# Performance work log

Hardware: AMD Instinct MI355X
Metric: run time of the kernel (lower is better)

Reference implementation:

```python
import jax, jax.numpy as jnp
import numpy as np

EPS = 1e-5
SLOPE = 0.2

def _knn_idx(x, k):
    # x: (B, N, C) -> idx (B, N, k), k nearest neighbors by squared L2 (incl. self)
    xx = jnp.sum(x * x, axis=-1)                      # (B, N)
    inner = jnp.einsum('bnc,bmc->bnm', x, x)          # (B, N, N)
    pd = -xx[:, :, None] + 2.0 * inner - xx[:, None, :]  # = -||xi-xj||^2
    return jax.lax.top_k(pd, k)[1]                    # (B, N, k)

def _bn(h, gamma, beta, axes):
    mean = jnp.mean(h, axis=axes, keepdims=True)
    var = jnp.var(h, axis=axes, keepdims=True)
    hn = (h - mean) * jax.lax.rsqrt(var + EPS)
    shape = [1] * h.ndim
    shape[-1] = h.shape[-1]
    return hn * gamma.reshape(shape) + beta.reshape(shape)

def _lrelu(h):
    return jnp.where(h >= 0, h, SLOPE * h)

def _edge_conv(x, k, W, gamma, beta):
    # x: (B, N, C); EdgeConv: knn -> gather -> [nb-x, x] -> 1x1 conv -> BN -> LeakyReLU -> max over k
    idx = _knn_idx(x, k)                                   # (B, N, k)
    nb = jax.vmap(lambda xb, ib: xb[ib])(x, idx)           # (B, N, k, C)
    xc = jnp.broadcast_to(x[:, :, None, :], nb.shape)
    feat = jnp.concatenate([nb - xc, xc], axis=-1)         # (B, N, k, 2C)
    h = jnp.einsum('bnkc,oc->bnko', feat, W)               # 1x1 conv, no bias
    h = _lrelu(_bn(h, gamma, beta, axes=(0, 1, 2)))
    return jnp.max(h, axis=2)                              # (B, N, O)

def setup_inputs() -> dict:
    key = jax.random.key(0)
    ks = jax.random.split(key, 16)
    B, N, feat_dim = 8, 2048, 1024
    def w(k_, o, i):
        # kaiming-uniform-ish init for 1x1 conv
        bound = 1.0 / np.sqrt(i)
        return jax.random.uniform(k_, (o, i), jnp.float32, -bound, bound)
    inp = {
        'x': jax.random.normal(ks[0], (B, N, 3), jnp.float32),
        'W1': w(ks[1], 64, 6),   'g1': jnp.ones((64,)),  'b1': jnp.zeros((64,)),
        'W2': w(ks[2], 64, 128), 'g2': jnp.ones((64,)),  'b2': jnp.zeros((64,)),
        'W3': w(ks[3], 128, 128),'g3': jnp.ones((128,)), 'b3': jnp.zeros((128,)),
        'W4': w(ks[4], 256, 256),'g4': jnp.ones((256,)), 'b4': jnp.zeros((256,)),
        'W5': w(ks[5], feat_dim, 512), 'g5': jnp.ones((feat_dim,)), 'b5': jnp.zeros((feat_dim,)),
        'k': 20,
    }
    return inp

def reference(x, W1, g1, b1, W2, g2, b2, W3, g3, b3, W4, g4, b4, W5, g5, b5, k):
    x1 = _edge_conv(x,  k, W1, g1, b1)   # (B, N, 64)
    x2 = _edge_conv(x1, k, W2, g2, b2)   # (B, N, 64)
    x3 = _edge_conv(x2, k, W3, g3, b3)   # (B, N, 128)
    x4 = _edge_conv(x3, k, W4, g4, b4)   # (B, N, 256)
    xc = jnp.concatenate([x1, x2, x3, x4], axis=-1)   # (B, N, 512)
    h = jnp.einsum('bnc,oc->bno', xc, W5)             # conv5 (1x1, no bias)
    h = _lrelu(_bn(h, g5, b5, axes=(0, 1)))           # BatchNorm1d + LeakyReLU
    out = jnp.max(h, axis=1)                          # global max over points
    return out[:, None, :]                            # (B, 1, feat_dim)
```

## Files before the change

kernel.cpp:

```cpp
#include <hip/hip_runtime.h>
#include <hip/hip_bf16.h>

#define BB 8
#define NN 2048
#define KK 20
#define KSEL 32
#define SCAP 256

typedef __attribute__((ext_vector_type(8))) short short8v;
typedef __attribute__((ext_vector_type(4))) float f32x4;

__global__ __launch_bounds__(256) void norms_k(const float* __restrict__ xin, int C, int stride,
                                               float* __restrict__ xx) {
  int p = blockIdx.x * 256 + threadIdx.x;
  if (p >= BB * NN) return;
  const float* r = xin + (size_t)p * stride;
  double s = 0.0;
  for (int c = 0; c < C; ++c) { double v = (double)r[c]; s += v * v; }
  xx[p] = (float)s;
}

__device__ __forceinline__ void bitsel_fallback(unsigned (&u)[32], int lane,
                                                int* __restrict__ outp)
{
  unsigned long long lmask = (1ull << lane) - 1ull;
  unsigned T = 0;
  bool exact = false;
  for (int b = 31; b >= 0; --b) {
    unsigned Tp = T | (1u << b);
    int cnt = 0;
#pragma unroll
    for (int q = 0; q < 32; ++q)
      cnt += __popcll(__ballot(u[q] >= Tp));
    if (cnt >= KSEL) {
      T = Tp;
      if (cnt == KSEL) { exact = true; break; }
    }
  }
  int cnt = 0;
#pragma unroll
  for (int q = 0; q < 32; ++q) {
    bool take = exact ? (u[q] >= T) : (u[q] > T);
    unsigned long long m = __ballot(take);
    if (take) outp[cnt + __popcll(m & lmask)] = lane + 64 * q;
    cnt += __popcll(m);
  }
  if (!exact) {
    int tneed = KSEL - cnt;
#pragma unroll
    for (int q = 0; q < 32; ++q) {
      if (tneed > 0) {
        bool eq = (u[q] == T);
        unsigned long long m = __ballot(eq);
        int before = __popcll(m & lmask);
        if (eq && before < tneed) outp[cnt + before] = lane + 64 * q;
        int c = __popcll(m);
        int used = c < tneed ? c : tneed;
        cnt += used; tneed -= used;
      }
    }
  }
}

__device__ __forceinline__ void thresel32(unsigned (&u)[32], int lane,
                                          unsigned* __restrict__ cv, int* __restrict__ ci,
                                          int* __restrict__ outp)
{
  unsigned long long lmask = (1ull << lane) - 1ull;
  unsigned lm = u[0];
#pragma unroll
  for (int q = 1; q < 32; ++q) lm = u[q] > lm ? u[q] : lm;
  unsigned T = 0;
  for (int b = 31; b >= 0; --b) {
    unsigned Tp = T | (1u << b);
    int c = __popcll(__ballot(lm >= Tp));
    if (c >= 32) { T = Tp; if (c == 32) break; }
  }
  int n0 = 0;
#pragma unroll
  for (int q = 0; q < 32; ++q) n0 += __popcll(__ballot(u[q] >= T));
  if (n0 <= SCAP) {
    int cnt = 0;
#pragma unroll
    for (int q = 0; q < 32; ++q) {
      bool take = u[q] >= T;
      unsigned long long m = __ballot(take);
      if (take) {
        int pos = cnt + __popcll(m & lmask);
        cv[pos] = u[q];
        ci[pos] = lane + 64 * q;
      }
      cnt += __popcll(m);
    }
    for (int i = lane; i < n0; i += 64) {
      unsigned vi = cv[i];
      int rank = 0;
      for (int j = 0; j < n0; ++j) {
        unsigned vj = cv[j];
        rank += (vj > vi || (vj == vi && j < i)) ? 1 : 0;
      }
      if (rank < KSEL) outp[rank] = ci[i];
    }
  } else {
    bitsel_fallback(u, lane, outp);
  }
}

__global__ __launch_bounds__(256) void knn3_k(const float* __restrict__ xin,
                                              int* __restrict__ cand)
{
  int t = threadIdx.x;
  int wv = t >> 6, lane = t & 63;
  const int BPB = NN / 16;
  int b = blockIdx.x / BPB;
  int p0 = (blockIdx.x % BPB) * 16;
  __shared__ float xs[3][NN];
  __shared__ unsigned cvs[4][SCAP];
  __shared__ int cis[4][SCAP];
  const float* xb = xin + (size_t)b * NN * 3;
  for (int e = t; e < NN * 3; e += 256) xs[e % 3][e / 3] = xb[e];
  __syncthreads();
  for (int rr = 0; rr < 4; ++rr) {
    int row = p0 + wv * 4 + rr;
    float xi0 = xs[0][row], xi1 = xs[1][row], xi2 = xs[2][row];
    unsigned u[32];
#pragma unroll
    for (int q = 0; q < 32; ++q) {
      int j = lane + 64 * q;
      float d0 = xi0 - xs[0][j], d1 = xi1 - xs[1][j], d2 = xi2 - xs[2][j];
      float v = -(d0 * d0 + d1 * d1 + d2 * d2);
      unsigned bb = __float_as_uint(v);
      u[q] = bb ^ (((unsigned)((int)bb >> 31)) | 0x80000000u);
    }
    thresel32(u, lane, cvs[wv], cis[wv], cand + ((size_t)(b * NN + row)) * KSEL);
  }
}

__global__ __launch_bounds__(512) void pdmfma_k(
    const unsigned short* __restrict__ Ah, const unsigned short* __restrict__ Al,
    int lda, long long az,
    float* __restrict__ D, const float* __restrict__ xx, int Kd)
{
  __shared__ unsigned short AsH[128 * 64];
  __shared__ unsigned short AsL[128 * 64];
  __shared__ unsigned short BsH[128 * 64];
  __shared__ unsigned short BsL[128 * 64];
  int z = blockIdx.z;
  const unsigned short* Ahb = Ah + az * z;
  const unsigned short* Alb = Al + az * z;
  float* Db = D + (size_t)NN * NN * z;
  const float* xxb = xx + (size_t)NN * z;
  int t = threadIdx.x;
  int w = t >> 6, lane = t & 63;
  int wm = w >> 2, wn = w & 3;
  int i0 = blockIdx.x * 128, j0 = blockIdx.y * 128;
  int fr = lane & 15, fg = lane >> 4;
  int srow = t >> 3;
  int scol = (t & 7) * 8;
  f32x4 acc[4][2] = {};
  for (int k0 = 0; k0 < Kd; k0 += 64) {
    short8v vah[2], valo[2], vbh[2], vbl[2];
#pragma unroll
    for (int rr = 0; rr < 2; ++rr) {
      int row = srow + rr * 64;
      vah[rr]  = *(const short8v*)(Ahb + (size_t)(i0 + row) * lda + k0 + scol);
      valo[rr] = *(const short8v*)(Alb + (size_t)(i0 + row) * lda + k0 + scol);
      vbh[rr]  = *(const short8v*)(Ahb + (size_t)(j0 + row) * lda + k0 + scol);
      vbl[rr]  = *(const short8v*)(Alb + (size_t)(j0 + row) * lda + k0 + scol);
    }
    __syncthreads();
#pragma unroll
    for (int rr = 0; rr < 2; ++rr) {
      int row = srow + rr * 64;
      int sw = (row * 64 + scol) ^ ((row & 7) << 3);
      *(short8v*)&AsH[sw] = vah[rr];
      *(short8v*)&AsL[sw] = valo[rr];
      *(short8v*)&BsH[sw] = vbh[rr];
      *(short8v*)&BsL[sw] = vbl[rr];
    }
    __syncthreads();
#pragma unroll
    for (int kk = 0; kk < 2; ++kk) {
      short8v ah[4], al[4], bh[2], bl[2];
      int kb = kk * 32 + fg * 8;
#pragma unroll
      for (int m = 0; m < 4; ++m) {
        int ar = wm * 64 + m * 16 + fr;
        int ai = (ar * 64 + kb) ^ ((ar & 7) << 3);
        ah[m] = *(const short8v*)&AsH[ai];
        al[m] = *(const short8v*)&AsL[ai];
      }
#pragma unroll
      for (int n = 0; n < 2; ++n) {
        int br = wn * 32 + n * 16 + fr;
        int bi = (br * 64 + kb) ^ ((br & 7) << 3);
        bh[n] = *(const short8v*)&BsH[bi];
        bl[n] = *(const short8v*)&BsL[bi];
      }
#pragma unroll
      for (int m = 0; m < 4; ++m)
#pragma unroll
        for (int n = 0; n < 2; ++n) {
          acc[m][n] = __builtin_amdgcn_mfma_f32_16x16x32_bf16(ah[m], bh[n], acc[m][n], 0, 0, 0);
          acc[m][n] = __builtin_amdgcn_mfma_f32_16x16x32_bf16(ah[m], bl[n], acc[m][n], 0, 0, 0);
          acc[m][n] = __builtin_amdgcn_mfma_f32_16x16x32_bf16(al[m], bh[n], acc[m][n], 0, 0, 0);
        }
    }
    __syncthreads();
  }
#pragma unroll
  for (int m = 0; m < 4; ++m) {
    float xi[4];
#pragma unroll
    for (int j = 0; j < 4; ++j) xi[j] = xxb[i0 + wm * 64 + m * 16 + fg * 4 + j];
#pragma unroll
    for (int n = 0; n < 2; ++n) {
      float xj = xxb[j0 + wn * 32 + n * 16 + fr];
#pragma unroll
      for (int j = 0; j < 4; ++j)
        Db[(size_t)(i0 + wm * 64 + m * 16 + fg * 4 + j) * NN +
           j0 + wn * 32 + n * 16 + fr] = 2.f * acc[m][n][j] - xi[j] - xj;
    }
  }
}

__global__ __launch_bounds__(512) void gemm_fb_k(
    const unsigned short* __restrict__ Ah, const unsigned short* __restrict__ Al, int lda,
    const unsigned short* __restrict__ Bh, const unsigned short* __restrict__ Bl, int ldb,
    float* __restrict__ C, int ldc, int Kd)
{
  __shared__ unsigned short AsH[128 * 64];
  __shared__ unsigned short AsL[128 * 64];
  __shared__ unsigned short BsH[128 * 64];
  __shared__ unsigned short BsL[128 * 64];
  int t = threadIdx.x;
  int w = t >> 6, lane = t & 63;
  int wm = w >> 2, wn = w & 3;
  int i0 = blockIdx.x * 128, j0 = blockIdx.y * 128;
  int fr = lane & 15, fg = lane >> 4;
  int srow = t >> 3;
  int scol = (t & 7) * 8;
  f32x4 acc[4][2] = {};
  for (int k0 = 0; k0 < Kd; k0 += 64) {
    short8v vah[2], valo[2], vbh[2], vbl[2];
#pragma unroll
    for (int rr = 0; rr < 2; ++rr) {
      int row = srow + rr * 64;
      vah[rr]  = *(const short8v*)(Ah + (size_t)(i0 + row) * lda + k0 + scol);
      valo[rr] = *(const short8v*)(Al + (size_t)(i0 + row) * lda + k0 + scol);
      vbh[rr]  = *(const short8v*)(Bh + (size_t)(j0 + row) * ldb + k0 + scol);
      vbl[rr]  = *(const short8v*)(Bl + (size_t)(j0 + row) * ldb + k0 + scol);
    }
    __syncthreads();
#pragma unroll
    for (int rr = 0; rr < 2; ++rr) {
      int row = srow + rr * 64;
      int sw = (row * 64 + scol) ^ ((row & 7) << 3);
      *(short8v*)&AsH[sw] = vah[rr];
      *(short8v*)&AsL[sw] = valo[rr];
      *(short8v*)&BsH[sw] = vbh[rr];
      *(short8v*)&BsL[sw] = vbl[rr];
    }
    __syncthreads();
#pragma unroll
    for (int kk = 0; kk < 2; ++kk) {
      short8v ah[4], al[4], bh[2], bl[2];
      int kb = kk * 32 + fg * 8;
#pragma unroll
      for (int m = 0; m < 4; ++m) {
        int ar = wm * 64 + m * 16 + fr;
        int ai = (ar * 64 + kb) ^ ((ar & 7) << 3);
        ah[m] = *(const short8v*)&AsH[ai];
        al[m] = *(const short8v*)&AsL[ai];
      }
#pragma unroll
      for (int n = 0; n < 2; ++n) {
        int br = wn * 32 + n * 16 + fr;
        int bi = (br * 64 + kb) ^ ((br & 7) << 3);
        bh[n] = *(const short8v*)&BsH[bi];
        bl[n] = *(const short8v*)&BsL[bi];
      }
#pragma unroll
      for (int m = 0; m < 4; ++m)
#pragma unroll
        for (int n = 0; n < 2; ++n) {
          acc[m][n] = __builtin_amdgcn_mfma_f32_16x16x32_bf16(ah[m], bh[n], acc[m][n], 0, 0, 0);
          acc[m][n] = __builtin_amdgcn_mfma_f32_16x16x32_bf16(ah[m], bl[n], acc[m][n], 0, 0, 0);
          acc[m][n] = __builtin_amdgcn_mfma_f32_16x16x32_bf16(al[m], bh[n], acc[m][n], 0, 0, 0);
        }
    }
    __syncthreads();
  }
#pragma unroll
  for (int m = 0; m < 4; ++m)
#pragma unroll
    for (int n = 0; n < 2; ++n)
#pragma unroll
      for (int j = 0; j < 4; ++j)
        C[(size_t)(i0 + wm * 64 + m * 16 + fg * 4 + j) * ldc +
          j0 + wn * 32 + n * 16 + fr] = acc[m][n][j];
}

__global__ __launch_bounds__(256) void topk32_k(const float* __restrict__ dist, int row0,
                                                int* __restrict__ cand)
{
  int wv = threadIdx.x >> 6;
  int row = blockIdx.x * 4 + wv;
  int lane = threadIdx.x & 63;
  const float* d = dist + (size_t)row * NN;
  unsigned u[32];
#pragma unroll
  for (int q = 0; q < 32; ++q) {
    unsigned b = __float_as_uint(d[lane + 64 * q]);
    unsigned mk = ((unsigned)((int)b >> 31)) | 0x80000000u;
    u[q] = b ^ mk;
  }
  __shared__ unsigned cvs[4][SCAP];
  __shared__ int cis[4][SCAP];
  thresel32(u, lane, cvs[wv], cis[wv], cand + (size_t)(row0 + row) * KSEL);
}

template <int C>
__global__ __launch_bounds__(256) void refine4_k(const float* __restrict__ xin, int stride,
                                                 const int* __restrict__ cand,
                                                 int* __restrict__ idxout)
{
  int t = threadIdx.x;
  int w = t >> 6, lane = t & 63;
  int p = blockIdx.x * 4 + w;
  int b = p >> 11;
  __shared__ float xi[4][C < 4 ? 4 : C];
  __shared__ double Lval[4][KSEL];
  __shared__ int Lidx[4][KSEL];
#pragma unroll
  for (int c = lane; c < C; c += 64) xi[w][c] = xin[(size_t)p * stride + c];
  __syncthreads();
  int m = lane >> 1, h = lane & 1;
  int q = cand[(size_t)p * KSEL + m];
  const float* xr = xin + (size_t)(b * NN + q) * stride;
  double s;
  if constexpr (C >= 8) {
    constexpr int half = C >> 1;
    int c0 = h * half;
    float4 v[half / 4];
#pragma unroll
    for (int i = 0; i < half / 4; ++i) v[i] = *(const float4*)(xr + c0 + 4 * i);
    double a0 = 0.0, a1 = 0.0, a2 = 0.0, a3 = 0.0;
#pragma unroll
    for (int i = 0; i < half / 4; ++i) {
      float4 xv = *(const float4*)(&xi[w][c0 + 4 * i]);
      double d0 = (double)xv.x - (double)v[i].x;
      double d1 = (double)xv.y - (double)v[i].y;
      double d2 = (double)xv.z - (double)v[i].z;
      double d3 = (double)xv.w - (double)v[i].w;
      a0 += d0 * d0; a1 += d1 * d1; a2 += d2 * d2; a3 += d3 * d3;
    }
    s = (a0 + a1) + (a2 + a3);
  } else {
    s = 0.0;
#pragma unroll
    for (int c = h; c < C; c += 2) {
      double d = (double)xi[w][c] - (double)xr[c];
      s += d * d;
    }
  }
  s += __shfl_xor(s, 1);
  if (h == 0) { Lval[w][m] = -s; Lidx[w][m] = q; }
  __syncthreads();
  int mm = lane & 31;
  double vm = Lval[w][mm];
  int im = Lidx[w][mm];
  int rank = 0;
#pragma unroll
  for (int j = 0; j < KSEL; ++j) {
    double vj = Lval[w][j];
    int ij = Lidx[w][j];
    rank += (vj > vm || (vj == vm && ij < im)) ? 1 : 0;
  }
  if (lane < 32 && rank < KK) idxout[(size_t)p * KK + rank] = im;
}

__global__ __launch_bounds__(256) void gemm128_k(
    const float* __restrict__ A, int lda,
    const float* __restrict__ Bm, int ldb,
    float* __restrict__ C, int ldc, int Kd)
{
  __shared__ float As[128 * 68];
  __shared__ float Bs[128 * 68];
  int i0 = blockIdx.x * 128;
  int j0 = blockIdx.y * 128;
  int t = threadIdx.x;
  int tx = t & 15, ty = t >> 4;
  float acc[8][8] = {};
  for (int k0 = 0; k0 < Kd; k0 += 64) {
    int kt = Kd - k0; if (kt > 64) kt = 64;
    if (kt == 64) {
      for (int e = t; e < 128 * 64; e += 256) {
        int i = e >> 6, c = e & 63;
        As[i * 68 + c] = A[(size_t)(i0 + i) * lda + k0 + c];
        Bs[i * 68 + c] = Bm[(size_t)(j0 + i) * ldb + k0 + c];
      }
    } else {
      for (int e = t; e < 128 * kt; e += 256) {
        int i = e / kt, c = e % kt;
        As[i * 68 + c] = A[(size_t)(i0 + i) * lda + k0 + c];
        Bs[i * 68 + c] = Bm[(size_t)(j0 + i) * ldb + k0 + c];
      }
    }
    __syncthreads();
    int kt4 = kt & ~3;
    for (int c = 0; c < kt4; c += 4) {
      float4 a4[8], b4[8];
#pragma unroll
      for (int r = 0; r < 8; ++r) a4[r] = *(const float4*)&As[(ty + 16 * r) * 68 + c];
#pragma unroll
      for (int q = 0; q < 8; ++q) b4[q] = *(const float4*)&Bs[(tx + 16 * q) * 68 + c];
#pragma unroll
      for (int r = 0; r < 8; ++r)
#pragma unroll
        for (int q = 0; q < 8; ++q)
          acc[r][q] += a4[r].x * b4[q].x + a4[r].y * b4[q].y +
                       a4[r].z * b4[q].z + a4[r].w * b4[q].w;
    }
    for (int c = kt4; c < kt; ++c) {
      float av[8], bv[8];
#pragma unroll
      for (int r = 0; r < 8; ++r) av[r] = As[(ty + 16 * r) * 68 + c];
#pragma unroll
      for (int q = 0; q < 8; ++q) bv[q] = Bs[(tx + 16 * q) * 68 + c];
#pragma unroll
      for (int r = 0; r < 8; ++r)
#pragma unroll
        for (int q = 0; q < 8; ++q) acc[r][q] += av[r] * bv[q];
    }
    __syncthreads();
  }
#pragma unroll
  for (int r = 0; r < 8; ++r)
#pragma unroll
    for (int q = 0; q < 8; ++q)
      C[(size_t)(i0 + ty + 16 * r) * ldc + j0 + tx + 16 * q] = acc[r][q];
}

__global__ __launch_bounds__(256) void gemm_c5_k(
    const unsigned short* __restrict__ A, int lda,
    const unsigned short* __restrict__ B, int ldb,
    float* __restrict__ pmx, float* __restrict__ pmn,
    double* __restrict__ psum, double* __restrict__ psq, int Kd)
{
  __shared__ unsigned short Asm[128 * 64];
  __shared__ unsigned short Bsm[128 * 64];
  int t = threadIdx.x;
  int w = t >> 6, lane = t & 63;
  int wm = w >> 1, wn = w & 1;
  int i0 = blockIdx.x * 128, j0 = blockIdx.y * 128;
  int fr = lane & 15, fg = lane >> 4;
  int srow = t >> 3;
  int scol = (t & 7) * 8;
  f32x4 acc[4][4] = {};
  for (int k0 = 0; k0 < Kd; k0 += 64) {
    short8v va[4], vb[4];
#pragma unroll
    for (int rr = 0; rr < 4; ++rr) {
      int row = srow + rr * 32;
      va[rr] = *(const short8v*)(A + (size_t)(i0 + row) * lda + k0 + scol);
      vb[rr] = *(const short8v*)(B + (size_t)(j0 + row) * ldb + k0 + scol);
    }
    __syncthreads();
#pragma unroll
    for (int rr = 0; rr < 4; ++rr) {
      int row = srow + rr * 32;
      int sw = (row * 64 + scol) ^ ((row & 7) << 3);
      *(short8v*)&Asm[sw] = va[rr];
      *(short8v*)&Bsm[sw] = vb[rr];
    }
    __syncthreads();
    short8v af[4][2], bf2[4][2];
#pragma unroll
    for (int m = 0; m < 4; ++m)
#pragma unroll
      for (int kk = 0; kk < 2; ++kk) {
        int ar = wm * 64 + m * 16 + fr, kb = kk * 32 + fg * 8;
        af[m][kk] = *(const short8v*)&Asm[(ar * 64 + kb) ^ ((ar & 7) << 3)];
        int br = wn * 64 + m * 16 + fr;
        bf2[m][kk] = *(const short8v*)&Bsm[(br * 64 + kb) ^ ((br & 7) << 3)];
      }
#pragma unroll
    for (int m = 0; m < 4; ++m)
#pragma unroll
      for (int n = 0; n < 4; ++n)
#pragma unroll
        for (int kk = 0; kk < 2; ++kk)
          acc[m][n] = __builtin_amdgcn_mfma_f32_16x16x32_bf16(af[m][kk], bf2[n][kk],
                                                              acc[m][n], 0, 0, 0);
  }
  float tmx[4], tmn[4];
  double ts[4], ts2[4];
#pragma unroll
  for (int n = 0; n < 4; ++n) {
    tmx[n] = -3.0e38f; tmn[n] = 3.0e38f; ts[n] = 0.0; ts2[n] = 0.0;
#pragma unroll
    for (int m = 0; m < 4; ++m)
#pragma unroll
      for (int j = 0; j < 4; ++j) {
        float v = acc[m][n][j];
        tmx[n] = fmaxf(tmx[n], v); tmn[n] = fminf(tmn[n], v);
        ts[n] += (double)v; ts2[n] += (double)v * (double)v;
      }
  }
#pragma unroll
  for (int off = 16; off < 64; off <<= 1)
#pragma unroll
    for (int n = 0; n < 4; ++n) {
      tmx[n] = fmaxf(tmx[n], __shfl_xor(tmx[n], off));
      tmn[n] = fminf(tmn[n], __shfl_xor(tmn[n], off));
      ts[n] += __shfl_xor(ts[n], off);
      ts2[n] += __shfl_xor(ts2[n], off);
    }
  __shared__ float smx[2][128], smn[2][128];
  __shared__ double ssm[2][128], ssq[2][128];
  __syncthreads();
  if (fg == 0) {
#pragma unroll
    for (int n = 0; n < 4; ++n) {
      int c = wn * 64 + n * 16 + fr;
      smx[wm][c] = tmx[n]; smn[wm][c] = tmn[n];
      ssm[wm][c] = ts[n];  ssq[wm][c] = ts2[n];
    }
  }
  __syncthreads();
  if (t < 128) {
    size_t base = (size_t)blockIdx.x * 1024 + j0 + t;
    pmx[base] = fmaxf(smx[0][t], smx[1][t]);
    pmn[base] = fminf(smn[0][t], smn[1][t]);
    psum[base] = ssm[0][t] + ssm[1][t];
    psq[base]  = ssq[0][t] + ssq[1][t];
  }
}

__global__ __launch_bounds__(256) void c5red_k(const float* __restrict__ pmx,
                                               const float* __restrict__ pmn,
                                               const double* __restrict__ psum,
                                               const double* __restrict__ psq,
                                               float* __restrict__ mx5, float* __restrict__ mn5,
                                               double* __restrict__ sums) {
  int gid = blockIdx.x * 256 + threadIdx.x;
  if (gid >= BB * 1024) return;
  int b = gid >> 10, o = gid & 1023;
  float mx = -3.0e38f, mn = 3.0e38f;
  double s = 0.0, s2 = 0.0;
#pragma unroll
  for (int ti = 0; ti < 16; ++ti) {
    size_t i = (size_t)(b * 16 + ti) * 1024 + o;
    mx = fmaxf(mx, pmx[i]); mn = fminf(mn, pmn[i]);
    s += psum[i]; s2 += psq[i];
  }
  mx5[gid] = mx; mn5[gid] = mn;
  atomicAdd(&sums[o], s);
  atomicAdd(&sums[1024 + o], s2);
}

__global__ __launch_bounds__(256) void wmod_k(const float* __restrict__ W, int O, int Cin,
                                              float* __restrict__ Wm,
                                              __hip_bfloat16* __restrict__ Wmh,
                                              __hip_bfloat16* __restrict__ Wml) {
  int i = blockIdx.x * 256 + threadIdx.x;
  if (i >= O * Cin) return;
  int o = i / Cin, c = i % Cin;
  float wl = W[(size_t)o * 2 * Cin + c];
  float wr = W[(size_t)o * 2 * Cin + Cin + c];
  float d = wr - wl;
  size_t iL = (size_t)o * Cin + c;
  size_t iR = (size_t)(O + o) * Cin + c;
  Wm[iL] = wl;
  Wm[iR] = d;
  __hip_bfloat16 hL = __float2bfloat16(wl);
  __hip_bfloat16 hR = __float2bfloat16(d);
  Wmh[iL] = hL; Wml[iL] = __float2bfloat16(wl - __bfloat162float(hL));
  Wmh[iR] = hR; Wml[iR] = __float2bfloat16(d - __bfloat162float(hR));
}

__global__ __launch_bounds__(256) void tobf16_k(const float* __restrict__ in, int n,
                                                __hip_bfloat16* __restrict__ outv) {
  int i = blockIdx.x * 256 + threadIdx.x;
  if (i < n) outv[i] = __float2bfloat16(in[i]);
}

template <int O, int PPB>
__global__ __launch_bounds__(256) void edgeep2_k(
    const float* __restrict__ z, const int* __restrict__ idx,
    float* __restrict__ hmax, float* __restrict__ hmin,
    double* __restrict__ partials)
{
  constexpr int G = 256 / O;
  constexpr int KSET = KK / G;
  const int ZW = 2 * O;
  int p0 = blockIdx.x * PPB;
  int t = threadIdx.x;
  int o = t % O, g = t / O;
  __shared__ int nb[PPB][KK];
  __shared__ float RM[2][PPB][256];
  __shared__ double RS[2][256];
  for (int e = t; e < PPB * KK; e += 256) nb[e / KK][e % KK] = idx[(size_t)p0 * KK + e];
  __syncthreads();
  double s = 0.0, s2 = 0.0;
  for (int pi = 0; pi < PPB; ++pi) {
    int p = p0 + pi;
    int b = p >> 11;
    float u = z[(size_t)p * ZW + O + o];
    float mx = -3.0e38f, mn = 3.0e38f;
#pragma unroll
    for (int kk = 0; kk < KSET; ++kk) {
      int q = nb[pi][g * KSET + kk];
      float y = z[((size_t)(b * NN + q)) * ZW + o];
      float h = u + y;
      mx = fmaxf(mx, h); mn = fminf(mn, h);
      s += (double)h; s2 += (double)h * (double)h;
    }
    RM[0][pi][t] = mx; RM[1][pi][t] = mn;
  }
  RS[0][t] = s; RS[1][t] = s2;
  __syncthreads();
  if (g == 0) {
    for (int pi = 0; pi < PPB; ++pi) {
      float mx = RM[0][pi][o], mn = RM[1][pi][o];
#pragma unroll
      for (int gg = 1; gg < G; ++gg) {
        mx = fmaxf(mx, RM[0][pi][o + gg * O]);
        mn = fminf(mn, RM[1][pi][o + gg * O]);
      }
      hmax[(size_t)(p0 + pi) * O + o] = mx;
      hmin[(size_t)(p0 + pi) * O + o] = mn;
    }
    double ss = s, ss2 = s2;
#pragma unroll
    for (int gg = 1; gg < G; ++gg) { ss += RS[0][o + gg * O]; ss2 += RS[1][o + gg * O]; }
    partials[(size_t)blockIdx.x * (2 * O) + o] = ss;
    partials[(size_t)blockIdx.x * (2 * O) + O + o] = ss2;
  }
}

__global__ __launch_bounds__(256) void redsums_k(const double* __restrict__ P, int nblk,
                                                 int twoO, double* __restrict__ sums) {
  int j = blockIdx.x;
  int t = threadIdx.x;
  double s = 0.0;
  for (int b = t; b < nblk; b += 256) s += P[(size_t)b * twoO + j];
  __shared__ double L[256];
  L[t] = s; __syncthreads();
  for (int st = 128; st > 0; st >>= 1) {
    if (t < st) L[t] += L[t + st];
    __syncthreads();
  }
  if (t == 0) {
    int O = twoO >> 1;
    sums[j < O ? j : 1024 + (j - O)] = L[0];
  }
}

__global__ __launch_bounds__(256) void mkscale_k(const double* __restrict__ sums,
                                                 const float* __restrict__ gam,
                                                 const float* __restrict__ bet,
                                                 int O, double invM,
                                                 float* __restrict__ scale,
                                                 float* __restrict__ shift) {
  int o = blockIdx.x * 256 + threadIdx.x;
  if (o >= O) return;
  double mean = sums[o] * invM;
  double var = sums[1024 + o] * invM - mean * mean;
  if (var < 0.0) var = 0.0;
  double r = 1.0 / sqrt(var + 1e-5);
  double s = (double)gam[o] * r;
  scale[o] = (float)s;
  shift[o] = (float)((double)bet[o] - mean * s);
}

__global__ __launch_bounds__(256) void apply_k(const float* __restrict__ hmax,
                                               const float* __restrict__ hmin,
                                               const float* __restrict__ scale,
                                               const float* __restrict__ shift,
                                               float* __restrict__ outb,
                                               __hip_bfloat16* __restrict__ outhi,
                                               __hip_bfloat16* __restrict__ outlo,
                                               int O, int ostride) {
  int gid = blockIdx.x * 256 + threadIdx.x;
  if (gid >= BB * NN * O) return;
  int p = gid / O, o = gid % O;
  float sc = scale[o];
  float v = (sc >= 0.f ? hmax[gid] : hmin[gid]) * sc + shift[o];
  float r = v >= 0.f ? v : 0.2f * v;
  __hip_bfloat16 hi = __float2bfloat16(r);
  float lo = r - __bfloat162float(hi);
  outb[(size_t)p * ostride + o] = r;
  outhi[(size_t)p * ostride + o] = hi;
  outlo[(size_t)p * ostride + o] = __float2bfloat16(lo);
}

__global__ __launch_bounds__(256) void c5out_k(const float* __restrict__ mx5,
                                               const float* __restrict__ mn5,
                                               const float* __restrict__ scale,
                                               const float* __restrict__ shift,
                                               float* __restrict__ out) {
  int i = blockIdx.x * 256 + threadIdx.x;
  if (i >= BB * 1024) return;
  int o = i % 1024;
  float sc = scale[o];
  float v = (sc >= 0.f ? mx5[i] : mn5[i]) * sc + shift[o];
  out[i] = v >= 0.f ? v : 0.2f * v;
}

extern "C" void kernel_launch(void* const* d_in, const int* in_sizes, int n_in,
                              void* d_out, int out_size, void* d_ws, size_t ws_size,
                              hipStream_t stream) {
  const float* x  = (const float*)d_in[0];
  const float* W1 = (const float*)d_in[1];
  const float* g1 = (const float*)d_in[2];
  const float* b1 = (const float*)d_in[3];
  const float* W2 = (const float*)d_in[4];
  const float* g2 = (const float*)d_in[5];
  const float* b2 = (const float*)d_in[6];
  const float* W3 = (const float*)d_in[7];
  const float* g3 = (const float*)d_in[8];
  const float* b3 = (const float*)d_in[9];
  const float* W4 = (const float*)d_in[10];
  const float* g4 = (const float*)d_in[11];
  const float* b4 = (const float*)d_in[12];
  const float* W5 = (const float*)d_in[13];
  const float* g5 = (const float*)d_in[14];
  const float* b5 = (const float*)d_in[15];
  float* out = (float*)d_out;

  char* base = (char*)d_ws;
  size_t off = 0;
  auto alloc = [&](size_t nbytes) -> void* {
    void* p = (void*)(base + off);
    off += (nbytes + 255) & ~(size_t)255;
    return p;
  };
  float*  xxf   = (float*)alloc((size_t)BB * NN * 4);
  int*    idx   = (int*)alloc((size_t)BB * NN * KK * 4);
  int*    cand  = (int*)alloc((size_t)BB * NN * KSEL * 4);
  float*  scale = (float*)alloc(1024 * 4);
  float*  shift = (float*)alloc(1024 * 4);
  double* sums  = (double*)alloc(2048 * 8);
  float*  mx5   = (float*)alloc(8192 * 4);
  float*  mn5   = (float*)alloc(8192 * 4);
  float*  pmx   = (float*)alloc((size_t)128 * 1024 * 4);
  float*  pmn   = (float*)alloc((size_t)128 * 1024 * 4);
  double* psum  = (double*)alloc((size_t)128 * 1024 * 8);
  double* psq   = (double*)alloc((size_t)128 * 1024 * 8);
  float*  wmod  = (float*)alloc((size_t)512 * 128 * 4);
  __hip_bfloat16* wmodh = (__hip_bfloat16*)alloc((size_t)512 * 128 * 2);
  __hip_bfloat16* wmodl = (__hip_bfloat16*)alloc((size_t)512 * 128 * 2);
  __hip_bfloat16* w5b = (__hip_bfloat16*)alloc((size_t)1024 * 512 * 2);
  double* parts = (double*)alloc((size_t)1024 * 512 * 8);
  float*  xcat  = (float*)alloc((size_t)BB * NN * 512 * 4);
  __hip_bfloat16* xcatb  = (__hip_bfloat16*)alloc((size_t)BB * NN * 512 * 2);
  __hip_bfloat16* xcatlo = (__hip_bfloat16*)alloc((size_t)BB * NN * 512 * 2);
  float*  hmax  = (float*)alloc((size_t)BB * NN * 256 * 4);
  float*  hmin  = (float*)alloc((size_t)BB * NN * 256 * 4);
  size_t zoff = off;
  float*  zar   = (float*)alloc((size_t)BB * NN * 1024 * 4);
  float*  dist  = (float*)zar;
  size_t avail = (ws_size > zoff) ? (ws_size - zoff) : ((size_t)BB * NN * 1024 * 4);
  int CB = (int)(avail / ((size_t)NN * NN * 4));
  if (CB > BB) CB = BB;
  if (CB < 1) CB = 1;

  const int PPB = 16;
  const int NBLK = BB * NN / PPB;

  auto run_layer = [&](const float* xin, const __hip_bfloat16* xinh,
                       const __hip_bfloat16* xinl, int stride, int Cin, int O,
                       const float* W, const float* gg, const float* bbeta,
                       int ooff, int variant) {
    if (Cin == 3) {
      knn3_k<<<BB * NN / 16, 256, 0, stream>>>(xin, cand);
    } else {
      norms_k<<<64, 256, 0, stream>>>(xin, Cin, stride, xxf);
      for (int b0 = 0; b0 < BB; b0 += CB) {
        int cb = BB - b0; if (cb > CB) cb = CB;
        dim3 gpd(16, 16, cb);
        pdmfma_k<<<gpd, 512, 0, stream>>>(
            (const unsigned short*)xinh + (size_t)b0 * NN * stride,
            (const unsigned short*)xinl + (size_t)b0 * NN * stride,
            stride, (long long)NN * stride,
            dist, xxf + (size_t)b0 * NN, Cin);
        topk32_k<<<cb * 512, 256, 0, stream>>>(dist, b0 * NN, cand);
      }
    }
    if (Cin == 3)
      refine4_k<3><<<BB * NN / 4, 256, 0, stream>>>(xin, stride, cand, idx);
    else if (Cin == 64)
      refine4_k<64><<<BB * NN / 4, 256, 0, stream>>>(xin, stride, cand, idx);
    else
      refine4_k<128><<<BB * NN / 4, 256, 0, stream>>>(xin, stride, cand, idx);
    wmod_k<<<(O * Cin + 255) / 256, 256, 0, stream>>>(W, O, Cin, wmod, wmodh, wmodl);
    if (Cin == 3) {
      dim3 gf(128, (2 * O) / 128, 1);
      gemm128_k<<<gf, 256, 0, stream>>>(xin, stride, wmod, Cin, zar, 2 * O, Cin);
    } else {
      dim3 gf(128, (2 * O) / 128, 1);
      gemm_fb_k<<<gf, 512, 0, stream>>>(
          (const unsigned short*)xinh, (const unsigned short*)xinl, stride,
          (const unsigned short*)wmodh, (const unsigned short*)wmodl, Cin,
          zar, 2 * O, Cin);
    }
    if (variant == 0)
      edgeep2_k<64, PPB><<<NBLK, 256, 0, stream>>>(zar, idx, hmax, hmin, parts);
    else if (variant == 1)
      edgeep2_k<128, PPB><<<NBLK, 256, 0, stream>>>(zar, idx, hmax, hmin, parts);
    else
      edgeep2_k<256, PPB><<<NBLK, 256, 0, stream>>>(zar, idx, hmax, hmin, parts);
    redsums_k<<<2 * O, 256, 0, stream>>>(parts, NBLK, 2 * O, sums);
    mkscale_k<<<(O + 255) / 256, 256, 0, stream>>>(
        sums, gg, bbeta, O, 1.0 / ((double)BB * NN * KK), scale, shift);
    apply_k<<<(BB * NN * O + 255) / 256, 256, 0, stream>>>(
        hmax, hmin, scale, shift, xcat + ooff, xcatb + ooff, xcatlo + ooff, O, 512);
  };

  run_layer(x,          nullptr,      nullptr,       3,   3,   64,  W1, g1, b1, 0,   0);
  run_layer(xcat + 0,   xcatb + 0,    xcatlo + 0,    512, 64,  64,  W2, g2, b2, 64,  0);
  run_layer(xcat + 64,  xcatb + 64,   xcatlo + 64,   512, 64,  128, W3, g3, b3, 128, 1);
  run_layer(xcat + 128, xcatb + 128,  xcatlo + 128,  512, 128, 256, W4, g4, b4, 256, 2);

  tobf16_k<<<(1024 * 512 + 255) / 256, 256, 0, stream>>>(W5, 1024 * 512, w5b);
  dim3 g5d(128, 8, 1);
  gemm_c5_k<<<g5d, 256, 0, stream>>>((const unsigned short*)xcatb, 512,
                                     (const unsigned short*)w5b, 512,
                                     pmx, pmn, psum, psq, 512);
  hipMemsetAsync(sums, 0, 2048 * 8, stream);
  c5red_k<<<32, 256, 0, stream>>>(pmx, pmn, psum, psq, mx5, mn5, sums);
  mkscale_k<<<4, 256, 0, stream>>>(sums, g5, b5, 1024, 1.0 / ((double)BB * NN),
                                   scale, shift);
  c5out_k<<<32, 256, 0, stream>>>(mx5, mn5, scale, shift, out);
}
```

Before: 573.1 us.

## Restructure edge epilogue to vectorized float4 per-thread channels over full k

The edge epilogue kernel is reorganised so each thread owns four consecutive channels and loops over all k neighbors, loading float4 rows instead of scalar floats. The shared-memory max/min reduction across neighbor groups goes away, and hmax/hmin are written directly as float4. Memory access becomes wider and the reduction stage is simpler, but each thread holds many double accumulators, which raises register pressure. It also needs PPB to be a multiple of the points-per-pass count.

```diff
diff --git a/kernel.cpp b/kernel.cpp
--- a/kernel.cpp
+++ b/kernel.cpp
@@ -587,56 +587,65 @@
 }
 
 template <int O, int PPB>
-__global__ __launch_bounds__(256) void edgeep2_k(
+__global__ __launch_bounds__(256) void edgeep3_k(
     const float* __restrict__ z, const int* __restrict__ idx,
     float* __restrict__ hmax, float* __restrict__ hmin,
     double* __restrict__ partials)
 {
-  constexpr int G = 256 / O;
-  constexpr int KSET = KK / G;
+  constexpr int TPP = O / 4;
+  constexpr int PTS = 256 / TPP;
   const int ZW = 2 * O;
   int p0 = blockIdx.x * PPB;
   int t = threadIdx.x;
-  int o = t % O, g = t / O;
+  int slot = t / TPP;
+  int lc = t % TPP;
+  int co = lc * 4;
   __shared__ int nb[PPB][KK];
-  __shared__ float RM[2][PPB][256];
-  __shared__ double RS[2][256];
+  __shared__ double SS[2][256][4];
   for (int e = t; e < PPB * KK; e += 256) nb[e / KK][e % KK] = idx[(size_t)p0 * KK + e];
   __syncthreads();
-  double s = 0.0, s2 = 0.0;
-  for (int pi = 0; pi < PPB; ++pi) {
+  double s0 = 0.0, s1 = 0.0, s2 = 0.0, s3 = 0.0;
+  double q0 = 0.0, q1 = 0.0, q2 = 0.0, q3 = 0.0;
+#pragma unroll
+  for (int it = 0; it < PPB / PTS; ++it) {
+    int pi = it * PTS + slot;
     int p = p0 + pi;
     int b = p >> 11;
-    float u = z[(size_t)p * ZW + O + o];
-    float mx = -3.0e38f, mn = 3.0e38f;
-#pragma unroll
-    for (int kk = 0; kk < KSET; ++kk) {
-      int q = nb[pi][g * KSET + kk];
-      float y = z[((size_t)(b * NN + q)) * ZW + o];
-      float h = u + y;
-      mx = fmaxf(mx, h); mn = fminf(mn, h);
-      s += (double)h; s2 += (double)h * (double)h;
-    }
-    RM[0][pi][t] = mx; RM[1][pi][t] = mn;
-  }
-  RS[0][t] = s; RS[1][t] = s2;
+    float4 u4 = *(const float4*)&z[(size_t)p * ZW + O + co];
+    float mx0 = -3.0e38f, mx1 = -3.0e38f, mx2 = -3.0e38f, mx3 = -3.0e38f;
+    float mn0 = 3.0e38f, mn1 = 3.0e38f, mn2 = 3.0e38f, mn3 = 3.0e38f;
+#pragma unroll
+    for (int kk = 0; kk < KK; ++kk) {
+      int q = nb[pi][kk];
+      float4 y4 = *(const float4*)&z[((size_t)(b * NN + q)) * ZW + co];
+      float h0 = u4.x + y4.x, h1 = u4.y + y4.y, h2 = u4.z + y4.z, h3 = u4.w + y4.w;
+      mx0 = fmaxf(mx0, h0); mn0 = fminf(mn0, h0);
+      mx1 = fmaxf(mx1, h1); mn1 = fminf(mn1, h1);
+      mx2 = fmaxf(mx2, h2); mn2 = fminf(mn2, h2);
+      mx3 = fmaxf(mx3, h3); mn3 = fminf(mn3, h3);
+      s0 += (double)h0; q0 += (double)h0 * (double)h0;
+      s1 += (double)h1; q1 += (double)h1 * (double)h1;
+      s2 += (double)h2; q2 += (double)h2 * (double)h2;
+      s3 += (double)h3; q3 += (double)h3 * (double)h3;
+    }
+    *(float4*)&hmax[(size_t)p * O + co] = float4{mx0, mx1, mx2, mx3};
+    *(float4*)&hmin[(size_t)p * O + co] = float4{mn0, mn1, mn2, mn3};
+  }
+  SS[0][t][0] = s0; SS[0][t][1] = s1; SS[0][t][2] = s2; SS[0][t][3] = s3;
+  SS[1][t][0] = q0; SS[1][t][1] = q1; SS[1][t][2] = q2; SS[1][t][3] = q3;
   __syncthreads();
-  if (g == 0) {
-    for (int pi = 0; pi < PPB; ++pi) {
-      float mx = RM[0][pi][o], mn = RM[1][pi][o];
-#pragma unroll
-      for (int gg = 1; gg < G; ++gg) {
-        mx = fmaxf(mx, RM[0][pi][o + gg * O]);
-        mn = fminf(mn, RM[1][pi][o + gg * O]);
-      }
-      hmax[(size_t)(p0 + pi) * O + o] = mx;
-      hmin[(size_t)(p0 + pi) * O + o] = mn;
-    }
-    double ss = s, ss2 = s2;
-#pragma unroll
-    for (int gg = 1; gg < G; ++gg) { ss += RS[0][o + gg * O]; ss2 += RS[1][o + gg * O]; }
-    partials[(size_t)blockIdx.x * (2 * O) + o] = ss;
-    partials[(size_t)blockIdx.x * (2 * O) + O + o] = ss2;
+  if (slot == 0) {
+    double a0 = 0.0, a1 = 0.0, a2 = 0.0, a3 = 0.0;
+    double b0 = 0.0, b1 = 0.0, b2 = 0.0, b3 = 0.0;
+#pragma unroll
+    for (int sl = 0; sl < PTS; ++sl) {
+      int tt = sl * TPP + lc;
+      a0 += SS[0][tt][0]; a1 += SS[0][tt][1]; a2 += SS[0][tt][2]; a3 += SS[0][tt][3];
+      b0 += SS[1][tt][0]; b1 += SS[1][tt][1]; b2 += SS[1][tt][2]; b3 += SS[1][tt][3];
+    }
+    double* pp = partials + (size_t)blockIdx.x * (2 * O);
+    pp[co + 0] = a0; pp[co + 1] = a1; pp[co + 2] = a2; pp[co + 3] = a3;
+    pp[O + co + 0] = b0; pp[O + co + 1] = b1; pp[O + co + 2] = b2; pp[O + co + 3] = b3;
   }
 }
 
@@ -807,11 +816,11 @@
           zar, 2 * O, Cin);
     }
     if (variant == 0)
-      edgeep2_k<64, PPB><<<NBLK, 256, 0, stream>>>(zar, idx, hmax, hmin, parts);
+      edgeep3_k<64, PPB><<<NBLK, 256, 0, stream>>>(zar, idx, hmax, hmin, parts);
     else if (variant == 1)
-      edgeep2_k<128, PPB><<<NBLK, 256, 0, stream>>>(zar, idx, hmax, hmin, parts);
+      edgeep3_k<128, PPB><<<NBLK, 256, 0, stream>>>(zar, idx, hmax, hmin, parts);
     else
-      edgeep2_k<256, PPB><<<NBLK, 256, 0, stream>>>(zar, idx, hmax, hmin, parts);
+      edgeep3_k<256, PPB><<<NBLK, 256, 0, stream>>>(zar, idx, hmax, hmin, parts);
     redsums_k<<<2 * O, 256, 0, stream>>>(parts, NBLK, 2 * O, sums);
     mkscale_k<<<(O + 255) / 256, 256, 0, stream>>>(
         sums, gg, bbeta, O, 1.0 / ((double)BB * NN * KK), scale, shift);
```

After: 575.8 us. No clear change (+0.5%).
